# Kernel optimization log

Hardware: AMD Instinct MI355X
Metric: run time of the kernel (lower is better)

## Reference

```python
import jax, jax.numpy as jnp
import numpy as np

D_POINTS, D_MODEL, K, B, N = 64, 128, 16, 2, 16384


def _linear(x, w, b=None):
    y = x @ w.T
    return y if b is None else y + b


def setup_inputs() -> dict:
    key = jax.random.key(0)
    ks = jax.random.split(key, 16)
    s = 0.02
    inp = {
        "new_xyz": jax.random.normal(ks[0], (B, N, 3), jnp.float32),
        "grouped_xyz": jax.random.normal(ks[1], (B, 3, N, K), jnp.float32),
        "grouped_idx": jax.random.randint(ks[2], (B, N, K), 0, N),
        "features": jax.random.normal(ks[3], (B, N, D_POINTS), jnp.float32),
        "fc1_w": jax.random.normal(ks[4], (D_MODEL, D_POINTS), jnp.float32) * s,
        "fc1_b": jnp.zeros((D_MODEL,), jnp.float32),
        "wq": jax.random.normal(ks[5], (D_MODEL, D_MODEL), jnp.float32) * s,
        "wk": jax.random.normal(ks[6], (D_MODEL, D_MODEL), jnp.float32) * s,
        "wv": jax.random.normal(ks[7], (D_MODEL, D_MODEL), jnp.float32) * s,
        "delta_w1": jax.random.normal(ks[8], (D_MODEL, 3), jnp.float32) * s,
        "delta_b1": jnp.zeros((D_MODEL,), jnp.float32),
        "delta_w2": jax.random.normal(ks[9], (D_MODEL, D_MODEL), jnp.float32) * s,
        "delta_b2": jnp.zeros((D_MODEL,), jnp.float32),
        "gamma_w1": jax.random.normal(ks[10], (D_MODEL, D_MODEL), jnp.float32) * s,
        "gamma_b1": jnp.zeros((D_MODEL,), jnp.float32),
        "gamma_w2": jax.random.normal(ks[11], (D_MODEL, D_MODEL), jnp.float32) * s,
        "gamma_b2": jnp.zeros((D_MODEL,), jnp.float32),
    }
    return inp


def reference(new_xyz, grouped_xyz, grouped_idx, features,
              fc1_w, fc1_b, wq, wk, wv,
              delta_w1, delta_b1, delta_w2, delta_b2,
              gamma_w1, gamma_b1, gamma_w2, gamma_b2):
    # x: [B,N,d_model]
    x = _linear(features, fc1_w, fc1_b)
    q = x @ wq.T                               # [B,N,d]
    kx = x @ wk.T                              # [B,N,d]
    vx = x @ wv.T                              # [B,N,d]
    gather = jax.vmap(lambda a, i: a[i])       # per-batch gather -> [B,N,K,d]
    k = gather(kx, grouped_idx)
    v = gather(vx, grouped_idx)
    # pos_enc: fc_delta(new_xyz[:,:,None] - grouped_xyz.permute(0,2,3,1))
    rel = new_xyz[:, :, None, :] - jnp.transpose(grouped_xyz, (0, 2, 3, 1))  # [B,N,K,3]
    pos_enc = _linear(jax.nn.relu(_linear(rel, delta_w1, delta_b1)), delta_w2, delta_b2)
    # attn: fc_gamma(q - k + pos_enc), softmax over neighbor axis
    h = q[:, :, None, :] - k + pos_enc
    attn = _linear(jax.nn.relu(_linear(h, gamma_w1, gamma_b1)), gamma_w2, gamma_b2)
    attn = jax.nn.softmax(attn / np.sqrt(D_MODEL).astype(np.float32), axis=-2)
    out = jnp.einsum('bmnf,bmnf->bmf', attn, v + pos_enc)
    return out
```

## Files before the change

### kernel.cpp

```cpp
#include <hip/hip_runtime.h>
#include <hip/hip_bf16.h>
#include <math.h>

#define BB   2
#define NPTS 16384
#define KNB  16
#define DPTS 64
#define DM   128

typedef float  f32x4  __attribute__((ext_vector_type(4)));
typedef short  bf16x8 __attribute__((ext_vector_type(8)));

__device__ __forceinline__ unsigned short f2bf(float f) {
    union { __hip_bfloat16 h; unsigned short u; } v;
    v.h = __float2bfloat16(f);
    return v.u;
}
__device__ __forceinline__ float bf2f(unsigned short h) {
    union { unsigned u; float f; } v; v.u = ((unsigned)h) << 16;
    return v.f;
}

#define WOFF_DW2  0
#define WOFF_GW1  16384
#define WOFF_GW2  32768
#define WOFF_WQ   49152
#define WOFF_WK   65536
#define WOFF_WV   81920
#define WOFF_FC1  98304
#define WTOT      106496

__global__ __launch_bounds__(256) void cvtw_kernel(
    const float* __restrict__ dw2, const float* __restrict__ gw1,
    const float* __restrict__ gw2, const float* __restrict__ wq,
    const float* __restrict__ wk, const float* __restrict__ wv,
    const float* __restrict__ fc1_w, unsigned short* __restrict__ wb)
{
    const int i = blockIdx.x * 256 + threadIdx.x;
    if (i >= WTOT) return;
    float v;
    if (i < WOFF_WQ) {
        const int which = i >> 14, off = i & 16383;
        v = (which == 0) ? dw2[off] : (which == 1) ? gw1[off] : gw2[off];
    } else if (i < WOFF_FC1) {
        const int j = i - WOFF_WQ;
        const int which = j >> 14, off = j & 16383;
        v = (which == 0) ? wq[off] : (which == 1) ? wk[off] : wv[off];
    } else {
        v = fc1_w[i - WOFF_FC1];
    }
    wb[i] = f2bf(v);
}

#define ABSTR 136

__device__ __forceinline__ void mfma_gemm(const unsigned short* __restrict__ AB,
                                          const unsigned short* __restrict__ Wb,
                                          int lane, int wbase, f32x4 acc[4][2])
{
    const int c = lane & 15, g = lane >> 4;
    bf16x8 Bf[2][4];
#pragma unroll
    for (int ct = 0; ct < 2; ++ct)
#pragma unroll
        for (int ks = 0; ks < 4; ++ks)
            Bf[ct][ks] = *(const bf16x8*)&Wb[(wbase + ct * 16 + c) * DM + ks * 32 + g * 8];
#pragma unroll
    for (int rt = 0; rt < 4; ++rt) {
        bf16x8 Af[4];
#pragma unroll
        for (int ks = 0; ks < 4; ++ks)
            Af[ks] = *(const bf16x8*)&AB[(rt * 16 + c) * ABSTR + ks * 32 + g * 8];
#pragma unroll
        for (int ct = 0; ct < 2; ++ct)
#pragma unroll
            for (int ks = 0; ks < 4; ++ks)
                acc[rt][ct] = __builtin_amdgcn_mfma_f32_16x16x32_bf16(
                    Af[ks], Bf[ct][ks], acc[rt][ct], 0, 0, 0);
    }
}

#define P_MT  64
#define FSTR  72

__global__ __launch_bounds__(256, 4) void proj_kernel(
    const float* __restrict__ features, const float* __restrict__ fc1_b,
    const unsigned short* __restrict__ wbf,
    unsigned short* __restrict__ qws, unsigned short* __restrict__ kws,
    unsigned short* __restrict__ vws)
{
    __shared__ __align__(16) unsigned short FB[P_MT * FSTR];
    __shared__ __align__(16) unsigned short XB[P_MT * ABSTR];

    const int tid  = threadIdx.x;
    const int lane = tid & 63;
    const int wave = tid >> 6;
    const int wbase = wave * 32;
    const int c  = lane & 15;
    const int g  = lane >> 4;
    const int g4 = g * 4;
    const size_t gp0 = (size_t)blockIdx.x * P_MT;

    for (int i = tid; i < P_MT * 8; i += 256) {
        const int r = i >> 3, o = i & 7;
        const float4 a = *(const float4*)&features[(gp0 + r) * DPTS + o * 8];
        const float4 b = *(const float4*)&features[(gp0 + r) * DPTS + o * 8 + 4];
        bf16x8 t;
        t[0] = (short)f2bf(a.x); t[1] = (short)f2bf(a.y);
        t[2] = (short)f2bf(a.z); t[3] = (short)f2bf(a.w);
        t[4] = (short)f2bf(b.x); t[5] = (short)f2bf(b.y);
        t[6] = (short)f2bf(b.z); t[7] = (short)f2bf(b.w);
        *(bf16x8*)&FB[r * FSTR + o * 8] = t;
    }
    __syncthreads();

    {
        const unsigned short* fw = wbf + WOFF_FC1;
        f32x4 acc[4][2];
#pragma unroll
        for (int rt = 0; rt < 4; ++rt)
#pragma unroll
            for (int ct = 0; ct < 2; ++ct) acc[rt][ct] = (f32x4)0.f;
        bf16x8 Bf[2][2];
#pragma unroll
        for (int ct = 0; ct < 2; ++ct)
#pragma unroll
            for (int ks = 0; ks < 2; ++ks)
                Bf[ct][ks] = *(const bf16x8*)&fw[(wbase + ct * 16 + c) * DPTS + ks * 32 + g * 8];
#pragma unroll
        for (int rt = 0; rt < 4; ++rt) {
            bf16x8 Af[2];
#pragma unroll
            for (int ks = 0; ks < 2; ++ks)
                Af[ks] = *(const bf16x8*)&FB[(rt * 16 + c) * FSTR + ks * 32 + g * 8];
#pragma unroll
            for (int ct = 0; ct < 2; ++ct)
#pragma unroll
                for (int ks = 0; ks < 2; ++ks)
                    acc[rt][ct] = __builtin_amdgcn_mfma_f32_16x16x32_bf16(
                        Af[ks], Bf[ct][ks], acc[rt][ct], 0, 0, 0);
        }
#pragma unroll
        for (int ct = 0; ct < 2; ++ct) {
            const int col = wbase + ct * 16 + c;
            const float bb = fc1_b[col];
#pragma unroll
            for (int rt = 0; rt < 4; ++rt)
#pragma unroll
                for (int rg = 0; rg < 4; ++rg)
                    XB[(rt * 16 + g4 + rg) * ABSTR + col] = f2bf(acc[rt][ct][rg] + bb);
        }
    }
    __syncthreads();

    const unsigned short* wmat[3] = { wbf + WOFF_WQ, wbf + WOFF_WK, wbf + WOFF_WV };
    unsigned short* outp[3] = { qws, kws, vws };
#pragma unroll
    for (int m = 0; m < 3; ++m) {
        f32x4 acc[4][2];
#pragma unroll
        for (int rt = 0; rt < 4; ++rt)
#pragma unroll
            for (int ct = 0; ct < 2; ++ct) acc[rt][ct] = (f32x4)0.f;
        mfma_gemm(XB, wmat[m], lane, wbase, acc);
#pragma unroll
        for (int ct = 0; ct < 2; ++ct) {
            const int col = wbase + ct * 16 + c;
#pragma unroll
            for (int rt = 0; rt < 4; ++rt)
#pragma unroll
                for (int rg = 0; rg < 4; ++rg)
                    outp[m][(gp0 + rt * 16 + g4 + rg) * DM + col] = f2bf(acc[rt][ct][rg]);
        }
    }
}

#define K2_PTS 4
#define K2_R   (K2_PTS * KNB)

__global__ __launch_bounds__(256, 4) void attn_kernel(
    const float* __restrict__ new_xyz, const float* __restrict__ grouped_xyz,
    const int* __restrict__ grouped_idx,
    const float* __restrict__ dw1, const float* __restrict__ db1,
    const float* __restrict__ db2,
    const float* __restrict__ gb1, const float* __restrict__ gb2,
    const unsigned short* __restrict__ wbf,
    const unsigned short* __restrict__ qws, const unsigned short* __restrict__ kws,
    const unsigned short* __restrict__ vws,
    float* __restrict__ out)
{
    __shared__ __align__(16) unsigned short AB[K2_R * ABSTR];
    __shared__ __align__(16) unsigned short SB[K2_R * ABSTR];
    __shared__ float REL[K2_R * 3];
    __shared__ int   IDX[K2_R];

    const int tid  = threadIdx.x;
    const int lane = tid & 63;
    const int wave = tid >> 6;
    const int wbase = wave * 32;
    const int c  = lane & 15;
    const int g  = lane >> 4;
    const int g4 = g * 4;
    const int rr = tid >> 4;
    const int o8 = (tid & 15) * 8;

    const int b   = blockIdx.x / (NPTS / K2_PTS);
    const int m0  = (blockIdx.x % (NPTS / K2_PTS)) * K2_PTS;
    const size_t gp0 = (size_t)b * NPTS + m0;
    const size_t bN  = (size_t)b * NPTS;
    const float SCL = 0.12751743342f;

    const unsigned short* dw2b = wbf + WOFF_DW2;
    const unsigned short* gw1b = wbf + WOFF_GW1;
    const unsigned short* gw2b = wbf + WOFF_GW2;

    float wr[24], bbv[8];
    {
        const float4* wsrc = (const float4*)&dw1[o8 * 3];
#pragma unroll
        for (int t = 0; t < 6; ++t) ((float4*)wr)[t] = wsrc[t];
        const float4* bsrc = (const float4*)&db1[o8];
        ((float4*)bbv)[0] = bsrc[0];
        ((float4*)bbv)[1] = bsrc[1];
    }

    if (tid < K2_R) {
        const int p = tid >> 4, j = tid & 15;
        const size_t m = gp0 + p;
        const int mi = m0 + p;
        IDX[tid] = grouped_idx[m * KNB + j];
#pragma unroll
        for (int cc = 0; cc < 3; ++cc)
            REL[tid * 3 + cc] = new_xyz[m * 3 + cc]
                              - grouped_xyz[(((size_t)b * 3 + cc) * NPTS + mi) * KNB + j];
    }
    __syncthreads();

    bf16x8 q8[4], k8[4];
#pragma unroll
    for (int it = 0; it < 4; ++it) {
        const int r = it * 16 + rr;
        q8[it] = *(const bf16x8*)&qws[(gp0 + it) * DM + o8];
        k8[it] = *(const bf16x8*)&kws[(bN + IDX[r]) * DM + o8];
    }

#pragma unroll
    for (int it = 0; it < 4; ++it) {
        const int r = it * 16 + rr;
        const float rx = REL[r * 3 + 0], ry = REL[r * 3 + 1], rz = REL[r * 3 + 2];
        bf16x8 t;
#pragma unroll
        for (int j = 0; j < 8; ++j) {
            float v = bbv[j];
            v = fmaf(rx, wr[j * 3 + 0], v);
            v = fmaf(ry, wr[j * 3 + 1], v);
            v = fmaf(rz, wr[j * 3 + 2], v);
            t[j] = (short)f2bf(fmaxf(v, 0.f));
        }
        *(bf16x8*)&AB[r * ABSTR + o8] = t;
    }
    __syncthreads();

    f32x4 posr[4][2];
    {
#pragma unroll
        for (int rt = 0; rt < 4; ++rt)
#pragma unroll
            for (int ct = 0; ct < 2; ++ct) posr[rt][ct] = (f32x4)0.f;
        mfma_gemm(AB, dw2b, lane, wbase, posr);
#pragma unroll
        for (int ct = 0; ct < 2; ++ct) {
            const int col = wbase + ct * 16 + c;
            const float bb = db2[col];
#pragma unroll
            for (int rt = 0; rt < 4; ++rt)
#pragma unroll
                for (int rg = 0; rg < 4; ++rg) {
                    posr[rt][ct][rg] += bb;
                    SB[(rt * 16 + g4 + rg) * ABSTR + col] = f2bf(posr[rt][ct][rg]);
                }
        }
    }
    __syncthreads();

#pragma unroll
    for (int it = 0; it < 4; ++it) {
        const int r = it * 16 + rr;
        const bf16x8 p8 = *(const bf16x8*)&SB[r * ABSTR + o8];
        bf16x8 t;
#pragma unroll
        for (int j = 0; j < 8; ++j) {
            const float hv = bf2f((unsigned short)q8[it][j])
                           - bf2f((unsigned short)k8[it][j])
                           + bf2f((unsigned short)p8[j]);
            t[j] = (short)f2bf(hv);
        }
        *(bf16x8*)&AB[r * ABSTR + o8] = t;
    }
    __syncthreads();

    {
        f32x4 acc[4][2];
#pragma unroll
        for (int rt = 0; rt < 4; ++rt)
#pragma unroll
            for (int ct = 0; ct < 2; ++ct) acc[rt][ct] = (f32x4)0.f;
        mfma_gemm(AB, gw1b, lane, wbase, acc);
#pragma unroll
        for (int ct = 0; ct < 2; ++ct) {
            const int col = wbase + ct * 16 + c;
            const float bb = gb1[col];
#pragma unroll
            for (int rt = 0; rt < 4; ++rt)
#pragma unroll
                for (int rg = 0; rg < 4; ++rg)
                    SB[(rt * 16 + g4 + rg) * ABSTR + col] = f2bf(fmaxf(acc[rt][ct][rg] + bb, 0.f));
        }
    }
    __syncthreads();

    f32x4 lg[4][2];
#pragma unroll
    for (int rt = 0; rt < 4; ++rt)
#pragma unroll
        for (int ct = 0; ct < 2; ++ct) lg[rt][ct] = (f32x4)0.f;
    mfma_gemm(SB, gw2b, lane, wbase, lg);
#pragma unroll
    for (int ct = 0; ct < 2; ++ct) {
        const int col = wbase + ct * 16 + c;
        const float bb = gb2[col];
#pragma unroll
        for (int rt = 0; rt < 4; ++rt)
#pragma unroll
            for (int rg = 0; rg < 4; ++rg)
                lg[rt][ct][rg] = (lg[rt][ct][rg] + bb) * SCL;
    }

#pragma unroll
    for (int rt = 0; rt < 4; ++rt)
#pragma unroll
    for (int ct = 0; ct < 2; ++ct) {
        const int col = wbase + ct * 16 + c;
        f32x4 l = lg[rt][ct];
        float mx = fmaxf(fmaxf(l[0], l[1]), fmaxf(l[2], l[3]));
        mx = fmaxf(mx, __shfl_xor(mx, 16));
        mx = fmaxf(mx, __shfl_xor(mx, 32));
        f32x4 e;
        e[0] = __builtin_amdgcn_exp2f(l[0] - mx);
        e[1] = __builtin_amdgcn_exp2f(l[1] - mx);
        e[2] = __builtin_amdgcn_exp2f(l[2] - mx);
        e[3] = __builtin_amdgcn_exp2f(l[3] - mx);
        float s = e[0] + e[1] + e[2] + e[3];
        s += __shfl_xor(s, 16);
        s += __shfl_xor(s, 32);
        float o = 0.f;
#pragma unroll
        for (int rg = 0; rg < 4; ++rg) {
            const int row = rt * 16 + g4 + rg;
            const float vv = bf2f(vws[(bN + IDX[row]) * DM + col]) + posr[rt][ct][rg];
            o = fmaf(e[rg], vv, o);
        }
        o += __shfl_xor(o, 16);
        o += __shfl_xor(o, 32);
        if (g == 0)
            out[(gp0 + rt) * DM + col] = o * __builtin_amdgcn_rcpf(s);
    }
}

extern "C" void kernel_launch(void* const* d_in, const int* in_sizes, int n_in,
                              void* d_out, int out_size, void* d_ws, size_t ws_size,
                              hipStream_t stream)
{
    const float* new_xyz     = (const float*)d_in[0];
    const float* grouped_xyz = (const float*)d_in[1];
    const int*   grouped_idx = (const int*)d_in[2];
    const float* features    = (const float*)d_in[3];
    const float* fc1_w = (const float*)d_in[4];
    const float* fc1_b = (const float*)d_in[5];
    const float* wq    = (const float*)d_in[6];
    const float* wk    = (const float*)d_in[7];
    const float* wv    = (const float*)d_in[8];
    const float* dw1   = (const float*)d_in[9];
    const float* db1   = (const float*)d_in[10];
    const float* dw2   = (const float*)d_in[11];
    const float* db2   = (const float*)d_in[12];
    const float* gw1   = (const float*)d_in[13];
    const float* gb1   = (const float*)d_in[14];
    const float* gw2   = (const float*)d_in[15];
    const float* gb2   = (const float*)d_in[16];
    float* out = (float*)d_out;

    unsigned short* ws = (unsigned short*)d_ws;
    const size_t npt = (size_t)BB * NPTS * DM;
    unsigned short* qws = ws;
    unsigned short* kws = ws + npt;
    unsigned short* vws = ws + 2 * npt;
    unsigned short* wbf = ws + 3 * npt;

    cvtw_kernel<<<(WTOT + 255) / 256, 256, 0, stream>>>(
        dw2, gw1, gw2, wq, wk, wv, fc1_w, wbf);

    proj_kernel<<<(BB * NPTS) / P_MT, 256, 0, stream>>>(
        features, fc1_b, wbf, qws, kws, vws);

    attn_kernel<<<(BB * NPTS) / K2_PTS, 256, 0, stream>>>(
        new_xyz, grouped_xyz, grouped_idx,
        dw1, db1, db2, gb1, gb2,
        wbf, qws, kws, vws, out);
}
```

Baseline: 167.0 us.

## Fold gamma_w1 into q/k/pos weights to drop one attention-stage GEMM pass

Result: slower. 180.9 us (+8.3%).

```diff
diff --git a/kernel.cpp b/kernel.cpp
--- a/kernel.cpp
+++ b/kernel.cpp
@@ -21,35 +21,53 @@
     return v.f;
 }
 
-#define WOFF_DW2  0
-#define WOFF_GW1  16384
-#define WOFF_GW2  32768
-#define WOFF_WQ   49152
-#define WOFF_WK   65536
-#define WOFF_WV   81920
-#define WOFF_FC1  98304
-#define WTOT      106496
-
-__global__ __launch_bounds__(256) void cvtw_kernel(
+#define WOFF_DW2CAT 0
+#define WOFF_GW2    32768
+#define WOFF_WQP    49152
+#define WOFF_WKP    65536
+#define WOFF_WV     81920
+#define WOFF_FC1    98304
+#define WTOT        106496
+
+__global__ __launch_bounds__(256) void prep_kernel(
     const float* __restrict__ dw2, const float* __restrict__ gw1,
     const float* __restrict__ gw2, const float* __restrict__ wq,
     const float* __restrict__ wk, const float* __restrict__ wv,
-    const float* __restrict__ fc1_w, unsigned short* __restrict__ wb)
+    const float* __restrict__ fc1_w, const float* __restrict__ db2,
+    const float* __restrict__ gb1,
+    unsigned short* __restrict__ wb, float* __restrict__ c1)
 {
-    const int i = blockIdx.x * 256 + threadIdx.x;
-    if (i >= WTOT) return;
-    float v;
-    if (i < WOFF_WQ) {
-        const int which = i >> 14, off = i & 16383;
-        v = (which == 0) ? dw2[off] : (which == 1) ? gw1[off] : gw2[off];
-    } else if (i < WOFF_FC1) {
-        const int j = i - WOFF_WQ;
-        const int which = j >> 14, off = j & 16383;
-        v = (which == 0) ? wq[off] : (which == 1) ? wk[off] : wv[off];
-    } else {
-        v = fc1_w[i - WOFF_FC1];
-    }
-    wb[i] = f2bf(v);
+    const int t = blockIdx.x * 256 + threadIdx.x;
+    if (t < 49152) {
+        const int mat = t >> 14, off = t & 16383;
+        const int r = off >> 7, k = off & 127;
+        const float* Bm = (mat == 0) ? dw2 : (mat == 1) ? wq : wk;
+        const float* arow = gw1 + r * DM;
+        float s = 0.f;
+#pragma unroll 4
+        for (int u = 0; u < DM; ++u)
+            s = fmaf(arow[u], Bm[u * DM + k], s);
+        const int dst = (mat == 0) ? (WOFF_DW2CAT + (DM + r) * DM + k)
+                      : (mat == 1) ? (WOFF_WQP + off) : (WOFF_WKP + off);
+        wb[dst] = f2bf(s);
+    } else if (t < 106496) {
+        const int j = t - 49152;
+        float v;
+        int dst;
+        if (j < 16384)      { v = dw2[j];  dst = WOFF_DW2CAT + j; }
+        else if (j < 32768) { v = gw2[j - 16384]; dst = WOFF_GW2 + (j - 16384); }
+        else if (j < 49152) { v = wv[j - 32768];  dst = WOFF_WV + (j - 32768); }
+        else                { v = fc1_w[j - 49152]; dst = WOFF_FC1 + (j - 49152); }
+        wb[dst] = f2bf(v);
+    } else if (t < 106624) {
+        const int i = t - 106496;
+        const float* arow = gw1 + i * DM;
+        float s = gb1[i];
+#pragma unroll 4
+        for (int u = 0; u < DM; ++u)
+            s = fmaf(arow[u], db2[u], s);
+        c1[i] = s;
+    }
 }
 
 #define ABSTR 136
@@ -153,7 +171,7 @@
     }
     __syncthreads();
 
-    const unsigned short* wmat[3] = { wbf + WOFF_WQ, wbf + WOFF_WK, wbf + WOFF_WV };
+    const unsigned short* wmat[3] = { wbf + WOFF_WQP, wbf + WOFF_WKP, wbf + WOFF_WV };
     unsigned short* outp[3] = { qws, kws, vws };
 #pragma unroll
     for (int m = 0; m < 3; ++m) {
@@ -183,8 +201,8 @@
     const int* __restrict__ grouped_idx,
     const float* __restrict__ dw1, const float* __restrict__ db1,
     const float* __restrict__ db2,
-    const float* __restrict__ gb1, const float* __restrict__ gb2,
-    const unsigned short* __restrict__ wbf,
+    const float* __restrict__ gb2,
+    const unsigned short* __restrict__ wbf, const float* __restrict__ c1,
     const unsigned short* __restrict__ qws, const unsigned short* __restrict__ kws,
     const unsigned short* __restrict__ vws,
     float* __restrict__ out)
@@ -210,9 +228,9 @@
     const size_t bN  = (size_t)b * NPTS;
     const float SCL = 0.12751743342f;
 
-    const unsigned short* dw2b = wbf + WOFF_DW2;
-    const unsigned short* gw1b = wbf + WOFF_GW1;
-    const unsigned short* gw2b = wbf + WOFF_GW2;
+    const unsigned short* dw2c0 = wbf + WOFF_DW2CAT;
+    const unsigned short* dw2c1 = wbf + WOFF_DW2CAT + DM * DM;
+    const unsigned short* gw2b  = wbf + WOFF_GW2;
 
     float wr[24], bbv[8];
     {
@@ -235,14 +253,6 @@
                               - grouped_xyz[(((size_t)b * 3 + cc) * NPTS + mi) * KNB + j];
     }
     __syncthreads();
-
-    bf16x8 q8[4], k8[4];
-#pragma unroll
-    for (int it = 0; it < 4; ++it) {
-        const int r = it * 16 + rr;
-        q8[it] = *(const bf16x8*)&qws[(gp0 + it) * DM + o8];
-        k8[it] = *(const bf16x8*)&kws[(bN + IDX[r]) * DM + o8];
-    }
 
 #pragma unroll
     for (int it = 0; it < 4; ++it) {
@@ -262,24 +272,39 @@
     __syncthreads();
 
     f32x4 posr[4][2];
-    {
+#pragma unroll
+    for (int rt = 0; rt < 4; ++rt)
+#pragma unroll
+        for (int ct = 0; ct < 2; ++ct) posr[rt][ct] = (f32x4)0.f;
+    mfma_gemm(AB, dw2c0, lane, wbase, posr);
+
+    f32x4 pw[4][2];
+#pragma unroll
+    for (int rt = 0; rt < 4; ++rt)
+#pragma unroll
+        for (int ct = 0; ct < 2; ++ct) pw[rt][ct] = (f32x4)0.f;
+    mfma_gemm(AB, dw2c1, lane, wbase, pw);
+
+    bf16x8 q8[4], k8[4];
+#pragma unroll
+    for (int it = 0; it < 4; ++it) {
+        const int r = it * 16 + rr;
+        q8[it] = *(const bf16x8*)&qws[(gp0 + it) * DM + o8];
+        k8[it] = *(const bf16x8*)&kws[(bN + IDX[r]) * DM + o8];
+    }
+
+#pragma unroll
+    for (int ct = 0; ct < 2; ++ct) {
+        const int col = wbase + ct * 16 + c;
+        const float bb = db2[col];
+        const float cc = c1[col];
 #pragma unroll
         for (int rt = 0; rt < 4; ++rt)
 #pragma unroll
-            for (int ct = 0; ct < 2; ++ct) posr[rt][ct] = (f32x4)0.f;
-        mfma_gemm(AB, dw2b, lane, wbase, posr);
-#pragma unroll
-        for (int ct = 0; ct < 2; ++ct) {
-            const int col = wbase + ct * 16 + c;
-            const float bb = db2[col];
-#pragma unroll
-            for (int rt = 0; rt < 4; ++rt)
-#pragma unroll
-                for (int rg = 0; rg < 4; ++rg) {
-                    posr[rt][ct][rg] += bb;
-                    SB[(rt * 16 + g4 + rg) * ABSTR + col] = f2bf(posr[rt][ct][rg]);
-                }
-        }
+            for (int rg = 0; rg < 4; ++rg) {
+                posr[rt][ct][rg] += bb;
+                SB[(rt * 16 + g4 + rg) * ABSTR + col] = f2bf(pw[rt][ct][rg] + cc);
+            }
     }
     __syncthreads();
 
@@ -293,38 +318,18 @@
             const float hv = bf2f((unsigned short)q8[it][j])
                            - bf2f((unsigned short)k8[it][j])
                            + bf2f((unsigned short)p8[j]);
-            t[j] = (short)f2bf(hv);
+            t[j] = (short)f2bf(fmaxf(hv, 0.f));
         }
         *(bf16x8*)&AB[r * ABSTR + o8] = t;
     }
     __syncthreads();
 
-    {
-        f32x4 acc[4][2];
-#pragma unroll
-        for (int rt = 0; rt < 4; ++rt)
-#pragma unroll
-            for (int ct = 0; ct < 2; ++ct) acc[rt][ct] = (f32x4)0.f;
-        mfma_gemm(AB, gw1b, lane, wbase, acc);
-#pragma unroll
-        for (int ct = 0; ct < 2; ++ct) {
-            const int col = wbase + ct * 16 + c;
-            const float bb = gb1[col];
-#pragma unroll
-            for (int rt = 0; rt < 4; ++rt)
-#pragma unroll
-                for (int rg = 0; rg < 4; ++rg)
-                    SB[(rt * 16 + g4 + rg) * ABSTR + col] = f2bf(fmaxf(acc[rt][ct][rg] + bb, 0.f));
-        }
-    }
-    __syncthreads();
-
     f32x4 lg[4][2];
 #pragma unroll
     for (int rt = 0; rt < 4; ++rt)
 #pragma unroll
         for (int ct = 0; ct < 2; ++ct) lg[rt][ct] = (f32x4)0.f;
-    mfma_gemm(SB, gw2b, lane, wbase, lg);
+    mfma_gemm(AB, gw2b, lane, wbase, lg);
 #pragma unroll
     for (int ct = 0; ct < 2; ++ct) {
         const int col = wbase + ct * 16 + c;
@@ -396,15 +401,16 @@
     unsigned short* kws = ws + npt;
     unsigned short* vws = ws + 2 * npt;
     unsigned short* wbf = ws + 3 * npt;
-
-    cvtw_kernel<<<(WTOT + 255) / 256, 256, 0, stream>>>(
-        dw2, gw1, gw2, wq, wk, wv, fc1_w, wbf);
+    float* c1 = (float*)(wbf + WTOT);
+
+    prep_kernel<<<(106624 + 255) / 256, 256, 0, stream>>>(
+        dw2, gw1, gw2, wq, wk, wv, fc1_w, db2, gb1, wbf, c1);
 
     proj_kernel<<<(BB * NPTS) / P_MT, 256, 0, stream>>>(
         features, fc1_b, wbf, qws, kws, vws);
 
     attn_kernel<<<(BB * NPTS) / K2_PTS, 256, 0, stream>>>(
         new_xyz, grouped_xyz, grouped_idx,
-        dw1, db1, db2, gb1, gb2,
-        wbf, qws, kws, vws, out);
-}
+        dw1, db1, db2, gb2,
+        wbf, c1, qws, kws, vws, out);
+}
```
